# Performance work log

Hardware: AMD Instinct MI355X
Metric: run time of the kernel (lower is better)

## Reference

```python
import jax, jax.numpy as jnp
import numpy as np

N_HEAD = 16
N_EMBD = 1024
HEAD_DIM = N_EMBD // N_HEAD
ROPE_BASE = 10000.0


def _rope_tables(T, dim):
    inv_freq = 1.0 / (ROPE_BASE ** (jnp.arange(0, dim, 2, dtype=jnp.float32) / dim))
    t = jnp.arange(T, dtype=jnp.float32)
    freqs = jnp.einsum('i,j->ij', t, inv_freq)          # [T, dim/2]
    emb = jnp.concatenate((freqs, freqs), axis=-1)       # [T, dim]
    return jnp.cos(emb), jnp.sin(emb)


def _rotate_half(x):
    x1, x2 = jnp.split(x, 2, axis=-1)
    return jnp.concatenate((-x2, x1), axis=-1)


def setup_inputs() -> dict:
    key = jax.random.key(0)
    k_x, k_wa, k_ba, k_wp, k_bp = jax.random.split(key, 5)
    B, T, C = 2, 2048, N_EMBD
    x = jax.random.normal(k_x, (B, T, C), dtype=jnp.float32)
    # torch Linear weights: [out, in]
    W_attn = jax.random.normal(k_wa, (3 * C, C), dtype=jnp.float32) * (1.0 / np.sqrt(C))
    b_attn = jax.random.normal(k_ba, (3 * C,), dtype=jnp.float32) * 0.01
    W_proj = jax.random.normal(k_wp, (C, C), dtype=jnp.float32) * (1.0 / np.sqrt(C))
    b_proj = jax.random.normal(k_bp, (C,), dtype=jnp.float32) * 0.01
    return {"x": x, "W_attn": W_attn, "b_attn": b_attn, "W_proj": W_proj, "b_proj": b_proj}


def reference(x, W_attn, b_attn, W_proj, b_proj):
    B, T, C = x.shape
    H, D = N_HEAD, HEAD_DIM
    qkv = jnp.einsum('btc,oc->bto', x, W_attn) + b_attn   # [B,T,3C]
    q, k, v = jnp.split(qkv, 3, axis=2)
    # [B,T,C] -> [B,H,T,D]
    q = q.reshape(B, T, H, D).transpose(0, 2, 1, 3)
    k = k.reshape(B, T, H, D).transpose(0, 2, 1, 3)
    v = v.reshape(B, T, H, D).transpose(0, 2, 1, 3)
    cos, sin = _rope_tables(T, D)                          # [T,D]
    q = q * cos + _rotate_half(q) * sin
    k = k * cos + _rotate_half(k) * sin
    att = jnp.einsum('bhqd,bhkd->bhqk', q, k) * (1.0 / np.sqrt(D))
    causal = jnp.tril(jnp.ones((T, T), dtype=bool))
    att = jnp.where(causal, att, -jnp.inf)
    att = jax.nn.softmax(att, axis=-1)
    y = jnp.einsum('bhqk,bhkd->bhqd', att, v)              # [B,H,T,D]
    y = y.transpose(0, 2, 1, 3).reshape(B, T, C)
    y = jnp.einsum('btc,oc->bto', y, W_proj) + b_proj
    return y
```

## Files before the change

kernel.cpp:

```cpp
#include <hip/hip_runtime.h>


typedef unsigned short u16;
typedef u16 u16x4 __attribute__((ext_vector_type(4)));
typedef u16 u16x8 __attribute__((ext_vector_type(8)));
typedef short s16x8 __attribute__((ext_vector_type(8)));
typedef float f32x4 __attribute__((ext_vector_type(4)));

#define T_SEQ 2048
#define C_EMB 1024
#define NH 16
#define HD 64

#define MFMA16(a, b, c) __builtin_amdgcn_mfma_f32_16x16x32_bf16(a, b, c, 0, 0, 0)

__device__ __forceinline__ u16 f2bf(float f) {
    union { float f; unsigned int i; } x; x.f = f;
    unsigned int r = x.i + 0x7fffu + ((x.i >> 16) & 1u);
    return (u16)(r >> 16);
}
__device__ __forceinline__ u16x4 pack4(f32x4 v) {
    u16x4 o;
#pragma unroll
    for (int j = 0; j < 4; ++j) o[j] = f2bf(v[j]);
    return o;
}

__global__ __launch_bounds__(256) void conv_k(const float* __restrict__ src, u16* __restrict__ dst, int n8) {
    int i = blockIdx.x * 256 + threadIdx.x;
    if (i >= n8) return;
    f32x4 a = ((const f32x4*)src)[i * 2];
    f32x4 b = ((const f32x4*)src)[i * 2 + 1];
    u16x8 o;
#pragma unroll
    for (int j = 0; j < 4; ++j) o[j] = f2bf(a[j]);
#pragma unroll
    for (int j = 0; j < 4; ++j) o[4 + j] = f2bf(b[j]);
    ((u16x8*)dst)[i] = o;
}

__global__ __launch_bounds__(256) void rope_tab_k(float2* __restrict__ tab) {
    int idx = blockIdx.x * 256 + threadIdx.x;
    int t = idx >> 5, j = idx & 31;
    float inv = __builtin_exp2f(-0.41524101186092f * (float)j);
    float s_, c_;
    sincosf((float)t * inv, &s_, &c_);
    tab[idx] = make_float2(c_, s_);
}

__global__ __launch_bounds__(256) void qkv_rope_k(const u16* __restrict__ xb, const u16* __restrict__ Wab,
                                                  const float* __restrict__ bias,
                                                  const float2* __restrict__ tab,
                                                  u16* __restrict__ qb, u16* __restrict__ kb,
                                                  u16* __restrict__ vt) {
    __shared__ u16 smem[2 * 128 * 72];
    u16* As = smem;
    u16* Bs = smem + 128 * 72;
    int tid = threadIdx.x;
    int n0 = blockIdx.x * 128, m0 = blockIdx.y * 128;
    int w = tid >> 6, lane = tid & 63, lr = lane & 15, quad = lane >> 4;
    int wr = w >> 1, wc = w & 1;
    f32x4 acc[4][4] = {};
    for (int kt = 0; kt < C_EMB; kt += 64) {
#pragma unroll
        for (int it = 0; it < 4; ++it) {
            int idx = it * 256 + tid;
            int row = idx >> 3, c8 = (idx & 7) << 3;
            *(s16x8*)&As[row * 72 + c8] = *(const s16x8*)(xb + (size_t)(m0 + row) * C_EMB + kt + c8);
            *(s16x8*)&Bs[row * 72 + c8] = *(const s16x8*)(Wab + (size_t)(n0 + row) * C_EMB + kt + c8);
        }
        __syncthreads();
#pragma unroll
        for (int ks = 0; ks < 64; ks += 32) {
            s16x8 af[4], bf[4];
#pragma unroll
            for (int i = 0; i < 4; ++i)
                af[i] = *(const s16x8*)&As[(wr * 64 + i * 16 + lr) * 72 + ks + quad * 8];
#pragma unroll
            for (int j = 0; j < 4; ++j)
                bf[j] = *(const s16x8*)&Bs[(wc * 64 + j * 16 + lr) * 72 + ks + quad * 8];
#pragma unroll
            for (int i = 0; i < 4; ++i)
#pragma unroll
                for (int j = 0; j < 4; ++j) acc[i][j] = MFMA16(af[i], bf[j], acc[i][j]);
        }
        __syncthreads();
    }
    int sec = n0 >> 10;
    float bv[4];
#pragma unroll
    for (int j = 0; j < 4; ++j) bv[j] = bias[n0 + wc * 64 + j * 16 + lr];

    int h0 = (n0 & 1023) >> 6;
    int b = m0 >> 11, tbase = m0 & 2047;
    if (sec == 2) {
        u16* Ct = smem;
#pragma unroll
        for (int i = 0; i < 4; ++i)
#pragma unroll
            for (int j = 0; j < 4; ++j) {
                f32x4 vv;
#pragma unroll
                for (int r = 0; r < 4; ++r) vv[r] = acc[i][j][r] + bv[j];
                int d = wc * 64 + j * 16 + lr;
                int m4 = wr * 64 + i * 16 + quad * 4;
                *(u16x4*)&Ct[d * 136 + m4] = pack4(vv);
            }
        __syncthreads();
        size_t hb = (size_t)(b * NH);
#pragma unroll
        for (int p = 0; p < 8; ++p) {
            int idx = p * 256 + tid;
            int d = idx >> 4, mc = (idx & 15) << 3;
            s16x8 vdat = *(const s16x8*)&Ct[d * 136 + mc];
            int h = h0 + (d >> 6), dd = d & 63;
            *(s16x8*)(vt + ((hb + h) * HD + dd) * T_SEQ + tbase + mc) = vdat;
        }
    } else {
        u16* dst = (sec == 0) ? qb : kb;
        float qs = (sec == 0) ? 0.125f : 1.0f;
        u16* Ct = smem;
#pragma unroll
        for (int i = 0; i < 4; ++i)
#pragma unroll
            for (int r = 0; r < 4; ++r) {
                int mrow = wr * 64 + i * 16 + quad * 4 + r;
                int t = (m0 + mrow) & 2047;
#pragma unroll
                for (int j = 0; j < 2; ++j) {
                    int d1 = j * 16 + lr;
                    float2 cs = tab[t * 32 + d1];
                    float v1 = acc[i][j][r] + bv[j];
                    float v2 = acc[i][j + 2][r] + bv[j + 2];
                    int n1 = wc * 64 + j * 16 + lr;
                    Ct[mrow * 136 + n1]      = f2bf((v1 * cs.x - v2 * cs.y) * qs);
                    Ct[mrow * 136 + n1 + 32] = f2bf((v2 * cs.x + v1 * cs.y) * qs);
                }
            }
        __syncthreads();
#pragma unroll
        for (int p = 0; p < 8; ++p) {
            int idx = p * 256 + tid;
            int mrow = idx >> 4, c = idx & 15;
            s16x8 vdat = *(const s16x8*)&Ct[mrow * 136 + c * 8];
            int h = h0 + (c >> 3), dd = (c & 7) << 3;
            *(s16x8*)(dst + ((size_t)(b * NH + h) * T_SEQ + tbase + mrow) * HD + dd) = vdat;
        }
    }
}

__global__ __launch_bounds__(256) void flash_k(const u16* __restrict__ qb, const u16* __restrict__ kb,
                                               const u16* __restrict__ vt, u16* __restrict__ yab) {
    __shared__ u16 Ks[64 * 72];
    __shared__ u16 Vs[64 * 72];
    __shared__ u16 Ps[4][32 * 72];
    int tid = threadIdx.x;
    int bx = blockIdx.x, by = blockIdx.y;
    int qt = (by < 16) ? (15 - bx) : bx;
    int bh = by;
    int w = tid >> 6, lane = tid & 63, lr = lane & 15, quad = lane >> 4;
    int q0 = qt * 128;
    const u16* qh = qb + (size_t)bh * T_SEQ * HD;
    const u16* kh = kb + (size_t)bh * T_SEQ * HD;
    const u16* vh = vt + (size_t)bh * HD * T_SEQ;

    s16x8 aq[2][2];
#pragma unroll
    for (int s = 0; s < 2; ++s)
#pragma unroll
        for (int ks = 0; ks < 2; ++ks)
            aq[s][ks] = *(const s16x8*)(qh + (size_t)(q0 + w * 32 + s * 16 + lr) * HD + ks * 32 + quad * 8);

    float m_i[2] = {-1e30f, -1e30f}, l_i[2] = {0.f, 0.f};
    f32x4 oacc[2][4] = {};

    int ktmax = 2 * qt + 1;
    for (int kt = 0; kt <= ktmax; ++kt) {
        int k0 = kt * 64;
#pragma unroll
        for (int p = 0; p < 2; ++p) {
            int idx = p * 256 + tid;
            int row = idx >> 3, c8 = (idx & 7) << 3;
            *(s16x8*)&Ks[row * 72 + c8] = *(const s16x8*)(kh + (size_t)(k0 + row) * HD + c8);
            *(s16x8*)&Vs[row * 72 + c8] = *(const s16x8*)(vh + (size_t)row * T_SEQ + k0 + c8);
        }
        __syncthreads();
        s16x8 ak[2][4];
#pragma unroll
        for (int ks = 0; ks < 2; ++ks)
#pragma unroll
            for (int tc = 0; tc < 4; ++tc)
                ak[ks][tc] = *(const s16x8*)&Ks[(tc * 16 + lr) * 72 + ks * 32 + quad * 8];

#pragma unroll
        for (int s = 0; s < 2; ++s) {
            int rbase = q0 + w * 32 + s * 16;
            if (k0 > rbase + 15) continue;
            f32x4 sacc[4] = {};
#pragma unroll
            for (int ks = 0; ks < 2; ++ks)
#pragma unroll
                for (int tc = 0; tc < 4; ++tc) sacc[tc] = MFMA16(ak[ks][tc], aq[s][ks], sacc[tc]);
            if (k0 + 63 > rbase) {
#pragma unroll
                for (int tc = 0; tc < 4; ++tc)
#pragma unroll
                    for (int r = 0; r < 4; ++r)
                        if (k0 + tc * 16 + quad * 4 + r > rbase + lr) sacc[tc][r] = -1e30f;
            }
            float mx = sacc[0][0];
#pragma unroll
            for (int tc = 0; tc < 4; ++tc)
#pragma unroll
                for (int r = 0; r < 4; ++r) mx = fmaxf(mx, sacc[tc][r]);
            mx = fmaxf(mx, __shfl_xor(mx, 16, 64));
            mx = fmaxf(mx, __shfl_xor(mx, 32, 64));
            float mn = fmaxf(m_i[s], mx);
            float alpha = __expf(m_i[s] - mn);
            m_i[s] = mn;
            float rs = 0.f;
#pragma unroll
            for (int tc = 0; tc < 4; ++tc)
#pragma unroll
                for (int r = 0; r < 4; ++r) {
                    float p = __expf(sacc[tc][r] - mn);
                    sacc[tc][r] = p;
                    rs += p;
                }
            rs += __shfl_xor(rs, 16, 64);
            rs += __shfl_xor(rs, 32, 64);
            l_i[s] = l_i[s] * alpha + rs;
#pragma unroll
            for (int tc = 0; tc < 4; ++tc)
                *(u16x4*)&Ps[w][(s * 16 + lr) * 72 + tc * 16 + quad * 4] = pack4(sacc[tc]);
#pragma unroll
            for (int tn = 0; tn < 4; ++tn)
#pragma unroll
                for (int r = 0; r < 4; ++r) oacc[s][tn][r] *= alpha;
#pragma unroll
            for (int ks = 0; ks < 2; ++ks) {
                s16x8 ap = *(const s16x8*)&Ps[w][(s * 16 + lr) * 72 + ks * 32 + quad * 8];
#pragma unroll
                for (int tn = 0; tn < 4; ++tn) {
                    s16x8 av = *(const s16x8*)&Vs[(tn * 16 + lr) * 72 + ks * 32 + quad * 8];
                    oacc[s][tn] = MFMA16(av, ap, oacc[s][tn]);
                }
            }
        }
        __syncthreads();
    }
    int b = bh >> 4, hh = bh & 15;
#pragma unroll
    for (int s = 0; s < 2; ++s) {
        float inv = 1.f / l_i[s];
        int t = q0 + w * 32 + s * 16 + lr;
        size_t base = ((size_t)b * T_SEQ + t) * C_EMB + hh * HD;
#pragma unroll
        for (int tn = 0; tn < 4; ++tn) {
            f32x4 vv;
#pragma unroll
            for (int r = 0; r < 4; ++r) vv[r] = oacc[s][tn][r] * inv;
            *(u16x4*)(yab + base + tn * 16 + quad * 4) = pack4(vv);
        }
    }
}

__global__ __launch_bounds__(256) void proj_k(const u16* __restrict__ ya, const u16* __restrict__ Wpb,
                                              const float* __restrict__ bias, float* __restrict__ out) {
    __shared__ u16 As[128 * 72];
    __shared__ u16 Bs[128 * 72];
    int tid = threadIdx.x;
    int n0 = blockIdx.x * 128, m0 = blockIdx.y * 128;
    int w = tid >> 6, lane = tid & 63, lr = lane & 15, quad = lane >> 4;
    int wr = w >> 1, wc = w & 1;
    f32x4 acc[4][4] = {};
    for (int kt = 0; kt < C_EMB; kt += 64) {
#pragma unroll
        for (int it = 0; it < 4; ++it) {
            int idx = it * 256 + tid;
            int row = idx >> 3, c8 = (idx & 7) << 3;
            *(s16x8*)&As[row * 72 + c8] = *(const s16x8*)(ya + (size_t)(m0 + row) * C_EMB + kt + c8);
            *(s16x8*)&Bs[row * 72 + c8] = *(const s16x8*)(Wpb + (size_t)(n0 + row) * C_EMB + kt + c8);
        }
        __syncthreads();
#pragma unroll
        for (int ks = 0; ks < 64; ks += 32) {
            s16x8 af[4], bf[4];
#pragma unroll
            for (int i = 0; i < 4; ++i)
                af[i] = *(const s16x8*)&As[(wr * 64 + i * 16 + lr) * 72 + ks + quad * 8];
#pragma unroll
            for (int j = 0; j < 4; ++j)
                bf[j] = *(const s16x8*)&Bs[(wc * 64 + j * 16 + lr) * 72 + ks + quad * 8];
#pragma unroll
            for (int i = 0; i < 4; ++i)
#pragma unroll
                for (int j = 0; j < 4; ++j) acc[i][j] = MFMA16(af[i], bf[j], acc[i][j]);
        }
        __syncthreads();
    }
    float bv[4];
#pragma unroll
    for (int j = 0; j < 4; ++j) bv[j] = bias[n0 + wc * 64 + j * 16 + lr];
#pragma unroll
    for (int i = 0; i < 4; ++i)
#pragma unroll
        for (int r = 0; r < 4; ++r) {
            int m = m0 + wr * 64 + i * 16 + quad * 4 + r;
#pragma unroll
            for (int j = 0; j < 4; ++j)
                out[(size_t)m * C_EMB + n0 + wc * 64 + j * 16 + lr] = acc[i][j][r] + bv[j];
        }
}

extern "C" void kernel_launch(void* const* d_in, const int* in_sizes, int n_in,
                              void* d_out, int out_size, void* d_ws, size_t ws_size,
                              hipStream_t stream) {
    const float *x = nullptr, *Wa = nullptr, *ba = nullptr, *Wp = nullptr, *bp = nullptr;
    for (int i = 0; i < n_in; ++i) {
        switch (in_sizes[i]) {
            case 4194304: x  = (const float*)d_in[i]; break;
            case 3145728: Wa = (const float*)d_in[i]; break;
            case 3072:    ba = (const float*)d_in[i]; break;
            case 1048576: Wp = (const float*)d_in[i]; break;
            case 1024:    bp = (const float*)d_in[i]; break;
            default: break;
        }
    }
    float* out = (float*)d_out;

    char* ws = (char*)d_ws;
    u16* qb     = (u16*)(ws);
    u16* kb     = (u16*)(ws + 8388608);
    u16* vt     = (u16*)(ws + 16777216);
    u16* yab    = (u16*)(ws + 25165824);
    float2* tab = (float2*)(ws + 33554432);
    u16* xb     = (u16*)(ws + 35651584);
    u16* Wab    = (u16*)(ws + 44040192);
    u16* Wpb    = (u16*)(ws + 50331648);

    conv_k<<<2048, 256, 0, stream>>>(x, xb, 524288);
    conv_k<<<1536, 256, 0, stream>>>(Wa, Wab, 393216);
    conv_k<<<512, 256, 0, stream>>>(Wp, Wpb, 131072);
    rope_tab_k<<<256, 256, 0, stream>>>(tab);
    qkv_rope_k<<<dim3(24, 32), 256, 0, stream>>>(xb, Wab, ba, tab, qb, kb, vt);
    flash_k<<<dim3(16, 32), 256, 0, stream>>>(qb, kb, vt, yab);
    proj_k<<<dim3(8, 32), 256, 0, stream>>>(yab, Wpb, bp, out);
}
```

Measured before the change: 223.3 us.

## Double-buffer K/V tiles, balance causal rows across waves, use exp2 with lazy rescale

The flash-attention kernel now double-buffers K/V tiles in shared memory and prefetches the next tile into registers during compute, which drops one barrier per iteration and hides global-load latency. Query rows are assigned to waves in a mirrored pattern so each wave gets an even share of the causal work. Softmax switches to exp2 with log2e folded into the Q scale. Rescaling of the max and accumulators is skipped unless the max grows by more than 8, trading some headroom against overflow for fewer multiplies. V fragments are also loaded once per tile instead of once per sub-row.

```diff
diff --git a/kernel.cpp b/kernel.cpp
--- a/kernel.cpp
+++ b/kernel.cpp
@@ -118,7 +118,7 @@
         }
     } else {
         u16* dst = (sec == 0) ? qb : kb;
-        float qs = (sec == 0) ? 0.125f : 1.0f;
+        float qs = (sec == 0) ? 0.18033688011112043f : 1.0f;
         u16* Ct = smem;
 #pragma unroll
         for (int i = 0; i < 4; ++i)
@@ -151,8 +151,8 @@
 
 __global__ __launch_bounds__(256) void flash_k(const u16* __restrict__ qb, const u16* __restrict__ kb,
                                                const u16* __restrict__ vt, u16* __restrict__ yab) {
-    __shared__ u16 Ks[64 * 72];
-    __shared__ u16 Vs[64 * 72];
+    __shared__ u16 Ks[2][64 * 72];
+    __shared__ u16 Vs[2][64 * 72];
     __shared__ u16 Ps[4][32 * 72];
     int tid = threadIdx.x;
     int bx = blockIdx.x, by = blockIdx.y;
@@ -164,37 +164,61 @@
     const u16* kh = kb + (size_t)bh * T_SEQ * HD;
     const u16* vh = vt + (size_t)bh * HD * T_SEQ;
 
+    int rb[2];
+    rb[0] = q0 + w * 16;
+    rb[1] = q0 + 112 - w * 16;
+
     s16x8 aq[2][2];
 #pragma unroll
     for (int s = 0; s < 2; ++s)
 #pragma unroll
         for (int ks = 0; ks < 2; ++ks)
-            aq[s][ks] = *(const s16x8*)(qh + (size_t)(q0 + w * 32 + s * 16 + lr) * HD + ks * 32 + quad * 8);
+            aq[s][ks] = *(const s16x8*)(qh + (size_t)(rb[s] + lr) * HD + ks * 32 + quad * 8);
+
+    int srow = tid >> 3, sc8 = (tid & 7) << 3;
 
     float m_i[2] = {-1e30f, -1e30f}, l_i[2] = {0.f, 0.f};
     f32x4 oacc[2][4] = {};
 
     int ktmax = 2 * qt + 1;
+    {
+        s16x8 kr0 = *(const s16x8*)(kh + (size_t)srow * HD + sc8);
+        s16x8 kr1 = *(const s16x8*)(kh + (size_t)(srow + 32) * HD + sc8);
+        s16x8 vr0 = *(const s16x8*)(vh + (size_t)srow * T_SEQ + sc8);
+        s16x8 vr1 = *(const s16x8*)(vh + (size_t)(srow + 32) * T_SEQ + sc8);
+        *(s16x8*)&Ks[0][srow * 72 + sc8] = kr0;
+        *(s16x8*)&Ks[0][(srow + 32) * 72 + sc8] = kr1;
+        *(s16x8*)&Vs[0][srow * 72 + sc8] = vr0;
+        *(s16x8*)&Vs[0][(srow + 32) * 72 + sc8] = vr1;
+    }
+    __syncthreads();
+
     for (int kt = 0; kt <= ktmax; ++kt) {
+        int cur = kt & 1;
         int k0 = kt * 64;
-#pragma unroll
-        for (int p = 0; p < 2; ++p) {
-            int idx = p * 256 + tid;
-            int row = idx >> 3, c8 = (idx & 7) << 3;
-            *(s16x8*)&Ks[row * 72 + c8] = *(const s16x8*)(kh + (size_t)(k0 + row) * HD + c8);
-            *(s16x8*)&Vs[row * 72 + c8] = *(const s16x8*)(vh + (size_t)row * T_SEQ + k0 + c8);
-        }
-        __syncthreads();
-        s16x8 ak[2][4];
+        bool pf = kt < ktmax;
+        s16x8 kr0, kr1, vr0, vr1;
+        if (pf) {
+            int kn = k0 + 64;
+            kr0 = *(const s16x8*)(kh + (size_t)(kn + srow) * HD + sc8);
+            kr1 = *(const s16x8*)(kh + (size_t)(kn + srow + 32) * HD + sc8);
+            vr0 = *(const s16x8*)(vh + (size_t)srow * T_SEQ + kn + sc8);
+            vr1 = *(const s16x8*)(vh + (size_t)(srow + 32) * T_SEQ + kn + sc8);
+        }
+        const u16* Kc = Ks[cur];
+        const u16* Vc = Vs[cur];
+        s16x8 ak[2][4], av[2][4];
 #pragma unroll
         for (int ks = 0; ks < 2; ++ks)
 #pragma unroll
-            for (int tc = 0; tc < 4; ++tc)
-                ak[ks][tc] = *(const s16x8*)&Ks[(tc * 16 + lr) * 72 + ks * 32 + quad * 8];
+            for (int tc = 0; tc < 4; ++tc) {
+                ak[ks][tc] = *(const s16x8*)&Kc[(tc * 16 + lr) * 72 + ks * 32 + quad * 8];
+                av[ks][tc] = *(const s16x8*)&Vc[(tc * 16 + lr) * 72 + ks * 32 + quad * 8];
+            }
 
 #pragma unroll
         for (int s = 0; s < 2; ++s) {
-            int rbase = q0 + w * 32 + s * 16;
+            int rbase = rb[s];
             if (k0 > rbase + 15) continue;
             f32x4 sacc[4] = {};
 #pragma unroll
@@ -208,44 +232,59 @@
                     for (int r = 0; r < 4; ++r)
                         if (k0 + tc * 16 + quad * 4 + r > rbase + lr) sacc[tc][r] = -1e30f;
             }
-            float mx = sacc[0][0];
-#pragma unroll
-            for (int tc = 0; tc < 4; ++tc)
-#pragma unroll
-                for (int r = 0; r < 4; ++r) mx = fmaxf(mx, sacc[tc][r]);
+            f32x4 mv = sacc[0];
+#pragma unroll
+            for (int tc = 1; tc < 4; ++tc)
+#pragma unroll
+                for (int r = 0; r < 4; ++r) mv[r] = fmaxf(mv[r], sacc[tc][r]);
+            float mx = fmaxf(fmaxf(mv[0], mv[1]), fmaxf(mv[2], mv[3]));
             mx = fmaxf(mx, __shfl_xor(mx, 16, 64));
             mx = fmaxf(mx, __shfl_xor(mx, 32, 64));
-            float mn = fmaxf(m_i[s], mx);
-            float alpha = __expf(m_i[s] - mn);
-            m_i[s] = mn;
-            float rs = 0.f;
+            float mo = m_i[s];
+            bool need = !__all(mx <= mo + 8.0f);
+            float alpha = 1.0f;
+            if (need) {
+                float mn = fmaxf(mo, mx);
+                alpha = __builtin_exp2f(mo - mn);
+                m_i[s] = mn;
+                l_i[s] *= alpha;
+            }
+            float mnow = m_i[s];
+            f32x4 rv = {0.f, 0.f, 0.f, 0.f};
 #pragma unroll
             for (int tc = 0; tc < 4; ++tc)
 #pragma unroll
                 for (int r = 0; r < 4; ++r) {
-                    float p = __expf(sacc[tc][r] - mn);
+                    float p = __builtin_exp2f(sacc[tc][r] - mnow);
                     sacc[tc][r] = p;
-                    rs += p;
+                    rv[r] += p;
                 }
+            float rs = (rv[0] + rv[1]) + (rv[2] + rv[3]);
             rs += __shfl_xor(rs, 16, 64);
             rs += __shfl_xor(rs, 32, 64);
-            l_i[s] = l_i[s] * alpha + rs;
+            l_i[s] += rs;
 #pragma unroll
             for (int tc = 0; tc < 4; ++tc)
                 *(u16x4*)&Ps[w][(s * 16 + lr) * 72 + tc * 16 + quad * 4] = pack4(sacc[tc]);
-#pragma unroll
-            for (int tn = 0; tn < 4; ++tn)
-#pragma unroll
-                for (int r = 0; r < 4; ++r) oacc[s][tn][r] *= alpha;
+            if (need) {
+#pragma unroll
+                for (int tn = 0; tn < 4; ++tn)
+#pragma unroll
+                    for (int r = 0; r < 4; ++r) oacc[s][tn][r] *= alpha;
+            }
 #pragma unroll
             for (int ks = 0; ks < 2; ++ks) {
                 s16x8 ap = *(const s16x8*)&Ps[w][(s * 16 + lr) * 72 + ks * 32 + quad * 8];
 #pragma unroll
-                for (int tn = 0; tn < 4; ++tn) {
-                    s16x8 av = *(const s16x8*)&Vs[(tn * 16 + lr) * 72 + ks * 32 + quad * 8];
-                    oacc[s][tn] = MFMA16(av, ap, oacc[s][tn]);
-                }
-            }
+                for (int tn = 0; tn < 4; ++tn) oacc[s][tn] = MFMA16(av[ks][tn], ap, oacc[s][tn]);
+            }
+        }
+        if (pf) {
+            int nx = cur ^ 1;
+            *(s16x8*)&Ks[nx][srow * 72 + sc8] = kr0;
+            *(s16x8*)&Ks[nx][(srow + 32) * 72 + sc8] = kr1;
+            *(s16x8*)&Vs[nx][srow * 72 + sc8] = vr0;
+            *(s16x8*)&Vs[nx][(srow + 32) * 72 + sc8] = vr1;
         }
         __syncthreads();
     }
@@ -253,7 +292,7 @@
 #pragma unroll
     for (int s = 0; s < 2; ++s) {
         float inv = 1.f / l_i[s];
-        int t = q0 + w * 32 + s * 16 + lr;
+        int t = rb[s] + lr;
         size_t base = ((size_t)b * T_SEQ + t) * C_EMB + hh * HD;
 #pragma unroll
         for (int tn = 0; tn < 4; ++tn) {
```

Result: no change. 222.5 us (-0.4%).
